# Kernel tuning notes

Hardware: AMD Instinct MI355X
Metric: run time of the kernel (lower is better)

Reference implementation:

```python
import jax, jax.numpy as jnp
import numpy as np

N = 100000   # nodes
D = 64       # node_emb_dim
R = 8        # num relations
E = 1600000  # edges (avg degree 16)


def setup_inputs() -> dict:
    key = jax.random.key(0)
    k1, k2, k3, k4, k5 = jax.random.split(key, 5)
    x = jax.random.normal(k1, (N, D), dtype=jnp.float32)
    edge_index = jax.random.randint(k2, (2, E), 0, N, dtype=jnp.int64)
    edge_type = jax.random.randint(k3, (E,), 0, R, dtype=jnp.int64)
    W_rel = jax.random.normal(k4, (R, D, D), dtype=jnp.float32) / np.sqrt(D)
    W_root = jax.random.normal(k5, (D, D), dtype=jnp.float32) / np.sqrt(D)
    bias = jnp.zeros((D,), dtype=jnp.float32)
    return {"x": x, "edge_index": edge_index, "edge_type": edge_type,
            "W_rel": W_rel, "W_root": W_root, "bias": bias}


def reference(x, edge_index, edge_type, W_rel, W_root, bias):
    # PyG RGCNConv: per-relation linear transform of source nodes,
    # mean-aggregated per (target node, relation), plus root transform + bias.
    n_nodes, d = x.shape
    n_rel = W_rel.shape[0]
    src, dst = edge_index[0], edge_index[1]

    # Transform every node under every relation once: [N, R, D]
    h_all = jnp.einsum('nd,rde->nre', x, W_rel)
    # Gather per-edge message: [E, D]
    msg = h_all[src, edge_type]

    # Per-(dst, relation) in-degree counts for mean normalization
    cnt = jnp.zeros((n_nodes, n_rel), dtype=x.dtype).at[dst, edge_type].add(1.0)
    norm = 1.0 / jnp.maximum(cnt[dst, edge_type], 1.0)  # [E]

    # Scatter-add normalized messages to target nodes
    agg = jnp.zeros((n_nodes, d), dtype=x.dtype).at[dst].add(msg * norm[:, None])

    out = agg + x @ W_root + bias
    return (out, edge_index, edge_type)
```

## Files before the change

kernel.cpp:

```cpp
#include <hip/hip_runtime.h>

#define DD 64
#define RR 8
#define KA 576
#define NT 18
#define NPART 8
#define ECH 2048
#define TILE 16

typedef short bf16x8 __attribute__((ext_vector_type(8)));
typedef float f32x4  __attribute__((ext_vector_type(4)));

__device__ __forceinline__ float bf2f(unsigned short u) {
    union { unsigned u; float f; } c; c.u = ((unsigned)u) << 16; return c.f;
}
__device__ __forceinline__ unsigned short f2bf(float f) {
    union { float f; unsigned u; } c; c.f = f;
    unsigned u = c.u;
    u += 0x7FFF + ((u >> 16) & 1);
    return (unsigned short)(u >> 16);
}

__global__ void k_xcast(const float* __restrict__ x, unsigned short* __restrict__ xb,
                        int N)
{
    int i = blockIdx.x * 256 + threadIdx.x;
    int total = (N + 1) * (DD / 4);
    if (i >= total) return;
    ushort4 o;
    if (i < N * (DD / 4)) {
        float4 f = ((const float4*)x)[i];
        o = make_ushort4(f2bf(f.x), f2bf(f.y), f2bf(f.z), f2bf(f.w));
    } else {
        o = make_ushort4(0, 0, 0, 0);
    }
    ((ushort4*)xb)[i] = o;
}

__global__ __launch_bounds__(256) void k_count_rank_echo(
    const int* __restrict__ ei, const int* __restrict__ et,
    int* __restrict__ cnt, unsigned* __restrict__ rr,
    float* __restrict__ out_ei, float* __restrict__ out_et, int E)
{
    const int base = blockIdx.x * ECH + threadIdx.x;
    int d[8], t[8], s[8], rk[8]; bool m[8];
    #pragma unroll
    for (int j = 0; j < 8; ++j) {
        int e = base + j * 256;
        m[j] = (e < E);
        d[j] = m[j] ? ei[E + e] : 0;
    }
    #pragma unroll
    for (int j = 0; j < 8; ++j) {
        int e = base + j * 256;
        if (m[j]) { t[j] = et[e]; s[j] = ei[e]; }
    }
    #pragma unroll
    for (int j = 0; j < 8; ++j)
        if (m[j]) rk[j] = atomicAdd(&cnt[(size_t)d[j] * RR + t[j]], 1);
    #pragma unroll
    for (int j = 0; j < 8; ++j) {
        int e = base + j * 256;
        if (m[j]) {
            rr[e] = (unsigned)rk[j] | ((unsigned)t[j] << 24);
            out_ei[e]     = (float)s[j];
            out_ei[E + e] = (float)d[j];
            out_et[e]     = (float)t[j];
        }
    }
}

__global__ __launch_bounds__(256) void k_alloc(
    const int* __restrict__ cnt, int* __restrict__ startv,
    int* __restrict__ start2, int* __restrict__ counter,
    int* __restrict__ sorted, int N)
{
    __shared__ int sdata[256];
    __shared__ int sbase;
    const int tid = threadIdx.x;
    const int n = blockIdx.x * 256 + tid;

    int deg = 0, deg8 = 0;
    int c[RR];
    if (n < N) {
        const int4* c4 = (const int4*)(cnt + (size_t)n * RR);
        int4 a = c4[0], b = c4[1];
        c[0]=a.x; c[1]=a.y; c[2]=a.z; c[3]=a.w;
        c[4]=b.x; c[5]=b.y; c[6]=b.z; c[7]=b.w;
        #pragma unroll
        for (int r = 0; r < RR; ++r) deg += c[r];
        deg8 = (deg + 7) & ~7;
    }
    sdata[tid] = deg8;
    __syncthreads();
    int v = deg8;
    #pragma unroll
    for (int off = 1; off < 256; off <<= 1) {
        int t = (tid >= off) ? sdata[tid - off] : 0;
        __syncthreads();
        v += t;
        sdata[tid] = v;
        __syncthreads();
    }
    if (tid == 255) sbase = atomicAdd(counter, v);
    __syncthreads();
    if (n < N) {
        int st = sbase + v - deg8;
        startv[n] = st;
        int h = st;
        #pragma unroll
        for (int r = 0; r < RR; ++r) { start2[(size_t)n * RR + r] = h; h += c[r]; }
        for (int j = deg; j < deg8; ++j) sorted[st + j] = N;
    }
}

__global__ __launch_bounds__(256) void k_scatter_part(
    const int* __restrict__ ei, const unsigned* __restrict__ rr,
    const int* __restrict__ start2, int* __restrict__ sorted, int E, int N)
{
    const int p    = blockIdx.x & (NPART - 1);
    const int sb   = blockIdx.x / NPART;
    const int dlo  = (int)((long long)N * p / NPART);
    const int dhi  = (int)((long long)N * (p + 1) / NPART);
    const int base = sb * ECH + threadIdx.x;

    int d[8]; bool m[8]; unsigned q[8]; int s[8], st[8];
    #pragma unroll
    for (int j = 0; j < 8; ++j) {
        int e = base + j * 256;
        d[j] = (e < E) ? ei[E + e] : -1;
    }
    #pragma unroll
    for (int j = 0; j < 8; ++j) m[j] = (d[j] >= dlo && d[j] < dhi);
    #pragma unroll
    for (int j = 0; j < 8; ++j) {
        int e = base + j * 256;
        if (m[j]) { q[j] = rr[e]; s[j] = ei[e]; }
    }
    #pragma unroll
    for (int j = 0; j < 8; ++j)
        if (m[j]) st[j] = start2[(size_t)d[j] * RR + (q[j] >> 24)];
    #pragma unroll
    for (int j = 0; j < 8; ++j)
        if (m[j]) sorted[st[j] + (q[j] & 0xFFFFFFu)] = s[j];
}

__global__ void k_packW(const float* __restrict__ Wrel, const float* __restrict__ Wroot,
                        unsigned short* __restrict__ Bh)
{
    int idx = blockIdx.x * 256 + threadIdx.x;
    if (idx >= NT * 4 * 64 * 8) return;
    int i    = idx & 7;
    int lane = (idx >> 3) & 63;
    int f    = (idx >> 9) & 3;
    int t    = idx >> 11;
    int k = t * 32 + (lane >> 4) * 8 + i;
    int d = f * 16 + (lane & 15);
    int r = k >> 6, kk = k & 63;
    float w = (r < RR) ? Wrel[((size_t)r * DD + kk) * DD + d]
                       : Wroot[(size_t)kk * DD + d];
    Bh[idx] = f2bf(w);
}

__global__ __launch_bounds__(256) void k_agg_mfma(
    const unsigned short* __restrict__ xb, const int* __restrict__ sorted,
    const int* __restrict__ startv, const int* __restrict__ cnt,
    const unsigned short* __restrict__ Bh, const float* __restrict__ bias,
    float* __restrict__ out, int N)
{
    __shared__ __align__(16) unsigned short As[TILE * KA];
    const int nb   = blockIdx.x * TILE;
    const int wv   = threadIdx.x >> 6;
    const int lane = threadIdx.x & 63;

    const int row0 = wv * 4;
    const int dst0 = nb + row0;
    const int nv   = min(4, N - dst0);
    if (nv > 0) {
        int cidx = lane & 31;
        if (cidx >= nv * 8) cidx = nv * 8 - 1;
        const int cv = cnt[(size_t)dst0 * RR + cidx];
        int sidx = lane & 3;
        if (sidx >= nv) sidx = nv - 1;
        const int sv = startv[dst0 + sidx];

        for (int i = 0; i < 4; ++i) {
            if (i >= nv) break;
            const int row = row0 + i;
            const int dst = dst0 + i;
            const int xsh = (row & 7) << 3;
            unsigned short* ao = As + row * KA;
            const int cb = i * 8;

            int deg = 0;
            #pragma unroll
            for (int r = 0; r < RR; ++r)
                deg += __builtin_amdgcn_readlane(cv, cb + r);
            const int deg8 = (deg + 7) & ~7;

            const int s0  = __builtin_amdgcn_readlane(sv, i);
            const int end = s0 + deg8;

            int   r      = 0;
            int   c_r    = __builtin_amdgcn_readlane(cv, cb);
            int   next_b = s0 + c_r;
            float cur    = 0.f;

            auto flush = [&]() {
                float inv = __builtin_amdgcn_rcpf(fmaxf((float)c_r, 1.f));
                ao[(r * DD + lane) ^ xsh] = f2bf(cur * inv);
                cur = 0.f;
                ++r;
                c_r = __builtin_amdgcn_readlane(cv, cb + (r & 7));
                next_b += c_r;
            };

            int e = s0;
            int wbase = s0;
            int vidx  = sorted[wbase + lane];
            while (e < end) {
                if (e - wbase >= 64) {
                    wbase = e;
                    vidx  = sorted[wbase + lane];
                }
                const int k    = e - wbase;
                const int take = min(end - e, 64 - k);
                for (int ii = 0; ii < take; ii += 8) {
                    int q0 = __builtin_amdgcn_readlane(vidx, k + ii + 0);
                    int q1 = __builtin_amdgcn_readlane(vidx, k + ii + 1);
                    int q2 = __builtin_amdgcn_readlane(vidx, k + ii + 2);
                    int q3 = __builtin_amdgcn_readlane(vidx, k + ii + 3);
                    int q4 = __builtin_amdgcn_readlane(vidx, k + ii + 4);
                    int q5 = __builtin_amdgcn_readlane(vidx, k + ii + 5);
                    int q6 = __builtin_amdgcn_readlane(vidx, k + ii + 6);
                    int q7 = __builtin_amdgcn_readlane(vidx, k + ii + 7);
                    unsigned short u0 = xb[(size_t)q0 * DD + lane];
                    unsigned short u1 = xb[(size_t)q1 * DD + lane];
                    unsigned short u2 = xb[(size_t)q2 * DD + lane];
                    unsigned short u3 = xb[(size_t)q3 * DD + lane];
                    unsigned short u4 = xb[(size_t)q4 * DD + lane];
                    unsigned short u5 = xb[(size_t)q5 * DD + lane];
                    unsigned short u6 = xb[(size_t)q6 * DD + lane];
                    unsigned short u7 = xb[(size_t)q7 * DD + lane];
                    const int base = e + ii;
                    while (base + 0 == next_b && r < RR) flush();
                    cur += bf2f(u0);
                    while (base + 1 == next_b && r < RR) flush();
                    cur += bf2f(u1);
                    while (base + 2 == next_b && r < RR) flush();
                    cur += bf2f(u2);
                    while (base + 3 == next_b && r < RR) flush();
                    cur += bf2f(u3);
                    while (base + 4 == next_b && r < RR) flush();
                    cur += bf2f(u4);
                    while (base + 5 == next_b && r < RR) flush();
                    cur += bf2f(u5);
                    while (base + 6 == next_b && r < RR) flush();
                    cur += bf2f(u6);
                    while (base + 7 == next_b && r < RR) flush();
                    cur += bf2f(u7);
                }
                e += take;
            }
            while (r < RR) flush();

            ao[(8 * DD + lane) ^ xsh] = xb[(size_t)dst * DD + lane];
        }
    }

    __syncthreads();

    const int rlo = lane & 15;
    const int kg  = lane >> 4;
    const int cf  = wv;
    const int row = rlo;
    const int xsh = (row & 7) << 3;

    f32x4 acc = {0.f,0.f,0.f,0.f};

    const unsigned short* arow = As + row * KA;
    #pragma unroll
    for (int t = 0; t < NT; ++t) {
        bf16x8 a = *(const bf16x8*)(arow + ((t * 32 + kg * 8) ^ xsh));
        bf16x8 b = *(const bf16x8*)(Bh + (size_t)t * 2048 + (size_t)cf * 512
                                       + lane * 8);
        acc = __builtin_amdgcn_mfma_f32_16x16x32_bf16(a, b, acc, 0, 0, 0);
    }

    const float bl = bias[rlo + cf * 16];
    const int orow = nb + kg * 4;
    #pragma unroll
    for (int j = 0; j < 4; ++j) {
        int rr2 = orow + j;
        if (rr2 < N) out[(size_t)rr2 * DD + rlo + cf * 16] = acc[j] + bl;
    }
}

extern "C" void kernel_launch(void* const* d_in, const int* in_sizes, int n_in,
                              void* d_out, int out_size, void* d_ws, size_t ws_size,
                              hipStream_t stream)
{
    const float* x     = (const float*)d_in[0];
    const int*   ei    = (const int*)d_in[1];
    const int*   et    = (const int*)d_in[2];
    const float* Wrel  = (const float*)d_in[3];
    const float* Wroot = (const float*)d_in[4];
    const float* bias  = (const float*)d_in[5];

    const int N = in_sizes[0] / DD;
    const int E = in_sizes[2];
    const int M = N * RR;

    float* out    = (float*)d_out;
    float* out_ei = out + (size_t)N * DD;
    float* out_et = out_ei + (size_t)2 * E;

    auto align = [](size_t v) { return (v + 255) & ~(size_t)255; };

    size_t p = 0;
    int* cnt = (int*)((char*)d_ws + p);              p += align((size_t)M * 4);
    int* counter = (int*)((char*)d_ws + p);
    size_t zero_bytes = p + 256;                     p += 256;
    int* startv = (int*)((char*)d_ws + p);           p += align((size_t)N * 4);
    int* start2 = (int*)((char*)d_ws + p);           p += align((size_t)M * 4);
    unsigned* rr = (unsigned*)((char*)d_ws + p);     p += align((size_t)E * 4);
    int* sorted = (int*)((char*)d_ws + p);           p += align(((size_t)E + 7*(size_t)N + 128) * 4);
    unsigned short* xb = (unsigned short*)((char*)d_ws + p); p += align(((size_t)N + 1) * DD * 2);
    unsigned short* Bh = (unsigned short*)((char*)d_ws + p); p += align((size_t)NT*4*64*8*2);

    hipMemsetAsync(d_ws, 0, zero_bytes, stream);

    const int nsb = (E + ECH - 1) / ECH;

    k_xcast <<<dim3(((N + 1) * (DD/4) + 255) / 256), 256, 0, stream>>>(x, xb, N);
    k_packW <<<dim3((NT*4*64*8 + 255) / 256), 256, 0, stream>>>(Wrel, Wroot, Bh);
    k_count_rank_echo <<<dim3(nsb), 256, 0, stream>>>(ei, et, cnt, rr,
                                                      out_ei, out_et, E);
    k_alloc <<<dim3((N + 255) / 256), 256, 0, stream>>>(cnt, startv, start2,
                                                        counter, sorted, N);
    k_scatter_part<<<dim3(nsb * NPART), 256, 0, stream>>>(ei, rr, start2, sorted, E, N);

    k_agg_mfma<<<dim3((N + TILE - 1) / TILE), 256, 0, stream>>>(
        xb, sorted, startv, cnt, Bh, bias, out, N);
}
```

Before: 212.4 us.

## Bucket edges into per-wave partition queues during counting; fuse prep kernels

The counting kernel now also sorts each wave's edges by destination partition with wave ballots. It writes packed 64-bit records (source, relation, destination, rank) into fixed-capacity per-wave, per-partition queues. The scatter kernel then reads only its own queue segments, instead of re-reading the full destination array once per partition plus the rank array. The x-to-bf16 cast and the weight-packing kernels are merged into one launch to save a launch. The cost is extra 64-bit queue writes and more ballot work in the counting kernel. Edges are silently dropped if a segment holds more than 160 entries, and the queue length is not clamped, so the scatter kernel would then read past its segment. Both cases are safe only for evenly spread destinations.

```diff
diff --git a/kernel.cpp b/kernel.cpp
--- a/kernel.cpp
+++ b/kernel.cpp
@@ -7,6 +7,7 @@
 #define NPART 8
 #define ECH 2048
 #define TILE 16
+#define SEGCAP 160
 
 typedef short bf16x8 __attribute__((ext_vector_type(8)));
 typedef float f32x4  __attribute__((ext_vector_type(4)));
@@ -21,28 +22,49 @@
     return (unsigned short)(u >> 16);
 }
 
-__global__ void k_xcast(const float* __restrict__ x, unsigned short* __restrict__ xb,
-                        int N)
-{
-    int i = blockIdx.x * 256 + threadIdx.x;
-    int total = (N + 1) * (DD / 4);
-    if (i >= total) return;
-    ushort4 o;
-    if (i < N * (DD / 4)) {
-        float4 f = ((const float4*)x)[i];
-        o = make_ushort4(f2bf(f.x), f2bf(f.y), f2bf(f.z), f2bf(f.w));
+__global__ __launch_bounds__(256) void k_prep(
+    const float* __restrict__ x, unsigned short* __restrict__ xb,
+    const float* __restrict__ Wrel, const float* __restrict__ Wroot,
+    unsigned short* __restrict__ Bh, int N, int xblocks)
+{
+    if ((int)blockIdx.x < xblocks) {
+        int i = blockIdx.x * 256 + threadIdx.x;
+        int total = (N + 1) * (DD / 4);
+        if (i >= total) return;
+        ushort4 o;
+        if (i < N * (DD / 4)) {
+            float4 f = ((const float4*)x)[i];
+            o = make_ushort4(f2bf(f.x), f2bf(f.y), f2bf(f.z), f2bf(f.w));
+        } else {
+            o = make_ushort4(0, 0, 0, 0);
+        }
+        ((ushort4*)xb)[i] = o;
     } else {
-        o = make_ushort4(0, 0, 0, 0);
-    }
-    ((ushort4*)xb)[i] = o;
+        int idx = (blockIdx.x - xblocks) * 256 + threadIdx.x;
+        if (idx >= NT * 4 * 64 * 8) return;
+        int i    = idx & 7;
+        int lane = (idx >> 3) & 63;
+        int f    = (idx >> 9) & 3;
+        int t    = idx >> 11;
+        int k = t * 32 + (lane >> 4) * 8 + i;
+        int d = f * 16 + (lane & 15);
+        int r = k >> 6, kk = k & 63;
+        float w = (r < RR) ? Wrel[((size_t)r * DD + kk) * DD + d]
+                           : Wroot[(size_t)kk * DD + d];
+        Bh[idx] = f2bf(w);
+    }
 }
 
 __global__ __launch_bounds__(256) void k_count_rank_echo(
     const int* __restrict__ ei, const int* __restrict__ et,
-    int* __restrict__ cnt, unsigned* __restrict__ rr,
-    float* __restrict__ out_ei, float* __restrict__ out_et, int E)
+    int* __restrict__ cnt, unsigned long long* __restrict__ q,
+    int* __restrict__ qlen, float* __restrict__ out_ei,
+    float* __restrict__ out_et, int E, unsigned pmagic)
 {
     const int base = blockIdx.x * ECH + threadIdx.x;
+    const int lane = threadIdx.x & 63;
+    const int gwid = blockIdx.x * 4 + (threadIdx.x >> 6);
+
     int d[8], t[8], s[8], rk[8]; bool m[8];
     #pragma unroll
     for (int j = 0; j < 8; ++j) {
@@ -62,11 +84,49 @@
     for (int j = 0; j < 8; ++j) {
         int e = base + j * 256;
         if (m[j]) {
-            rr[e] = (unsigned)rk[j] | ((unsigned)t[j] << 24);
             out_ei[e]     = (float)s[j];
             out_ei[E + e] = (float)d[j];
             out_et[e]     = (float)t[j];
         }
+    }
+
+    int run0=0,run1=0,run2=0,run3=0,run4=0,run5=0,run6=0,run7=0;
+    unsigned long long* qw = q + (size_t)gwid * NPART * SEGCAP;
+    #pragma unroll
+    for (int j = 0; j < 8; ++j) {
+        int pj = m[j]
+            ? (int)(((unsigned long long)(unsigned)d[j] * pmagic) >> 32)
+            : -1;
+        unsigned long long k0 = __ballot(pj == 0);
+        unsigned long long k1 = __ballot(pj == 1);
+        unsigned long long k2 = __ballot(pj == 2);
+        unsigned long long k3 = __ballot(pj == 3);
+        unsigned long long k4 = __ballot(pj == 4);
+        unsigned long long k5 = __ballot(pj == 5);
+        unsigned long long k6 = __ballot(pj == 6);
+        unsigned long long k7 = __ballot(pj == 7);
+        unsigned long long km =
+            (pj==0)?k0:(pj==1)?k1:(pj==2)?k2:(pj==3)?k3:
+            (pj==4)?k4:(pj==5)?k5:(pj==6)?k6:k7;
+        int bb =
+            (pj==0)?run0:(pj==1)?run1:(pj==2)?run2:(pj==3)?run3:
+            (pj==4)?run4:(pj==5)?run5:(pj==6)?run6:run7;
+        int off = __popcll(km & ((1ull << lane) - 1ull));
+        if (pj >= 0 && bb + off < SEGCAP) {
+            unsigned lo = (unsigned)s[j] | ((unsigned)t[j]  << 20);
+            unsigned hi = (unsigned)d[j] | ((unsigned)rk[j] << 20);
+            qw[(size_t)pj * SEGCAP + bb + off] =
+                ((unsigned long long)hi << 32) | lo;
+        }
+        run0 += __popcll(k0); run1 += __popcll(k1);
+        run2 += __popcll(k2); run3 += __popcll(k3);
+        run4 += __popcll(k4); run5 += __popcll(k5);
+        run6 += __popcll(k6); run7 += __popcll(k7);
+    }
+    if (lane == 0) {
+        int* ql = qlen + (size_t)gwid * NPART;
+        ql[0]=run0; ql[1]=run1; ql[2]=run2; ql[3]=run3;
+        ql[4]=run4; ql[5]=run5; ql[6]=run6; ql[7]=run7;
     }
 }
 
@@ -114,52 +174,24 @@
     }
 }
 
-__global__ __launch_bounds__(256) void k_scatter_part(
-    const int* __restrict__ ei, const unsigned* __restrict__ rr,
-    const int* __restrict__ start2, int* __restrict__ sorted, int E, int N)
+__global__ __launch_bounds__(256) void k_scatter_seg(
+    const unsigned long long* __restrict__ q, const int* __restrict__ qlen,
+    const int* __restrict__ start2, int* __restrict__ sorted, int nwaves)
 {
     const int p    = blockIdx.x & (NPART - 1);
-    const int sb   = blockIdx.x / NPART;
-    const int dlo  = (int)((long long)N * p / NPART);
-    const int dhi  = (int)((long long)N * (p + 1) / NPART);
-    const int base = sb * ECH + threadIdx.x;
-
-    int d[8]; bool m[8]; unsigned q[8]; int s[8], st[8];
-    #pragma unroll
-    for (int j = 0; j < 8; ++j) {
-        int e = base + j * 256;
-        d[j] = (e < E) ? ei[E + e] : -1;
-    }
-    #pragma unroll
-    for (int j = 0; j < 8; ++j) m[j] = (d[j] >= dlo && d[j] < dhi);
-    #pragma unroll
-    for (int j = 0; j < 8; ++j) {
-        int e = base + j * 256;
-        if (m[j]) { q[j] = rr[e]; s[j] = ei[e]; }
-    }
-    #pragma unroll
-    for (int j = 0; j < 8; ++j)
-        if (m[j]) st[j] = start2[(size_t)d[j] * RR + (q[j] >> 24)];
-    #pragma unroll
-    for (int j = 0; j < 8; ++j)
-        if (m[j]) sorted[st[j] + (q[j] & 0xFFFFFFu)] = s[j];
-}
-
-__global__ void k_packW(const float* __restrict__ Wrel, const float* __restrict__ Wroot,
-                        unsigned short* __restrict__ Bh)
-{
-    int idx = blockIdx.x * 256 + threadIdx.x;
-    if (idx >= NT * 4 * 64 * 8) return;
-    int i    = idx & 7;
-    int lane = (idx >> 3) & 63;
-    int f    = (idx >> 9) & 3;
-    int t    = idx >> 11;
-    int k = t * 32 + (lane >> 4) * 8 + i;
-    int d = f * 16 + (lane & 15);
-    int r = k >> 6, kk = k & 63;
-    float w = (r < RR) ? Wrel[((size_t)r * DD + kk) * DD + d]
-                       : Wroot[(size_t)kk * DD + d];
-    Bh[idx] = f2bf(w);
+    const int grp  = blockIdx.x / NPART;
+    const int gwid = grp * 4 + (threadIdx.x >> 6);
+    const int lane = threadIdx.x & 63;
+    if (gwid >= nwaves) return;
+    const int seg = gwid * NPART + p;
+    const int len = qlen[seg];
+    const unsigned long long* qs = q + (size_t)seg * SEGCAP;
+    for (int i = lane; i < len; i += 64) {
+        unsigned long long v = qs[i];
+        int cell = (int)((v >> 32) & 0xFFFFFu) * RR + (int)((v >> 20) & 7u);
+        int pos  = start2[cell] + (int)(v >> 52);
+        sorted[pos] = (int)(v & 0xFFFFFu);
+    }
 }
 
 __global__ __launch_bounds__(256) void k_agg_mfma(
@@ -317,29 +349,38 @@
 
     auto align = [](size_t v) { return (v + 255) & ~(size_t)255; };
 
+    const int nsb    = (E + ECH - 1) / ECH;
+    const int nwaves = nsb * 4;
+    const int ngrp   = (nwaves + 3) / 4;
+
     size_t p = 0;
     int* cnt = (int*)((char*)d_ws + p);              p += align((size_t)M * 4);
     int* counter = (int*)((char*)d_ws + p);
     size_t zero_bytes = p + 256;                     p += 256;
     int* startv = (int*)((char*)d_ws + p);           p += align((size_t)N * 4);
     int* start2 = (int*)((char*)d_ws + p);           p += align((size_t)M * 4);
-    unsigned* rr = (unsigned*)((char*)d_ws + p);     p += align((size_t)E * 4);
+    unsigned long long* q = (unsigned long long*)((char*)d_ws + p);
+    p += align((size_t)nwaves * NPART * SEGCAP * 8);
+    int* qlen = (int*)((char*)d_ws + p);             p += align((size_t)nwaves * NPART * 4);
     int* sorted = (int*)((char*)d_ws + p);           p += align(((size_t)E + 7*(size_t)N + 128) * 4);
     unsigned short* xb = (unsigned short*)((char*)d_ws + p); p += align(((size_t)N + 1) * DD * 2);
     unsigned short* Bh = (unsigned short*)((char*)d_ws + p); p += align((size_t)NT*4*64*8*2);
 
     hipMemsetAsync(d_ws, 0, zero_bytes, stream);
 
-    const int nsb = (E + ECH - 1) / ECH;
-
-    k_xcast <<<dim3(((N + 1) * (DD/4) + 255) / 256), 256, 0, stream>>>(x, xb, N);
-    k_packW <<<dim3((NT*4*64*8 + 255) / 256), 256, 0, stream>>>(Wrel, Wroot, Bh);
-    k_count_rank_echo <<<dim3(nsb), 256, 0, stream>>>(ei, et, cnt, rr,
-                                                      out_ei, out_et, E);
-    k_alloc <<<dim3((N + 255) / 256), 256, 0, stream>>>(cnt, startv, start2,
-                                                        counter, sorted, N);
-    k_scatter_part<<<dim3(nsb * NPART), 256, 0, stream>>>(ei, rr, start2, sorted, E, N);
-
+    unsigned pmagic = (unsigned)((((unsigned long long)NPART << 32) + N - 1) / N);
+
+    const int xblocks = ((N + 1) * (DD / 4) + 255) / 256;
+    const int wblocks = (NT * 4 * 64 * 8 + 255) / 256;
+
+    k_prep<<<dim3(xblocks + wblocks), 256, 0, stream>>>(
+        x, xb, Wrel, Wroot, Bh, N, xblocks);
+    k_count_rank_echo<<<dim3(nsb), 256, 0, stream>>>(
+        ei, et, cnt, q, qlen, out_ei, out_et, E, pmagic);
+    k_alloc<<<dim3((N + 255) / 256), 256, 0, stream>>>(
+        cnt, startv, start2, counter, sorted, N);
+    k_scatter_seg<<<dim3(ngrp * NPART), 256, 0, stream>>>(
+        q, qlen, start2, sorted, nwaves);
     k_agg_mfma<<<dim3((N + TILE - 1) / TILE), 256, 0, stream>>>(
         xb, sorted, startv, cnt, Bh, bias, out, N);
 }
```

New measurement: 193.2 us. 1.1x faster.
